# Kernel optimization log

Measured on AMD Instinct MI355X. Metric: run time of the kernel, lower is better.

Reference implementation:

```python
import jax, jax.numpy as jnp
import numpy as np
import math

B, L, C_IN = 64, 3168, 64
D_MODEL, K = 512, 16  # K = cycle_length (kernel width == stride)
W = L // K            # 198 output tokens from deform conv


def _positional(S, d, dtype):
    # PositionalEmbedding buffer, rows [0, S)
    pos = jnp.arange(S, dtype=jnp.float32)[:, None]
    div = jnp.exp(jnp.arange(0, d, 2, dtype=jnp.float32) * (-math.log(10000.0) / d))
    pe = jnp.zeros((S, d), jnp.float32)
    pe = pe.at[:, 0::2].set(jnp.sin(pos * div))
    pe = pe.at[:, 1::2].set(jnp.cos(pos * div))
    return pe.astype(dtype)


def setup_inputs() -> dict:
    key = jax.random.key(0)
    ks = jax.random.split(key, 6)
    fan_in = C_IN * K
    std = math.sqrt(2.0 / (1 + 0.01 ** 2) / fan_in)  # kaiming_normal, leaky_relu fan_in
    return {
        "x": jax.random.normal(ks[0], (B, L, C_IN), jnp.float32),
        "w_off": jax.random.normal(ks[1], (2 * K, C_IN, K), jnp.float32) * std,
        "b_off": jax.random.normal(ks[2], (2 * K,), jnp.float32) * 0.02,
        "w_def": jax.random.normal(ks[3], (D_MODEL, C_IN, K), jnp.float32) * std,
        "b_def": jax.random.normal(ks[4], (D_MODEL,), jnp.float32) * 0.02,
        "cls_token": jax.random.normal(ks[5], (1, 1, D_MODEL), jnp.float32),
    }


def _gather_cols(xt, idx, L_):
    # xt: (B, C, L); idx: (B, K, W) int32 -> (B, C, K, W), zero out-of-bounds
    b, c = xt.shape[0], xt.shape[1]
    valid = (idx >= 0) & (idx < L_)
    idxc = jnp.clip(idx, 0, L_ - 1).reshape(b, 1, -1)
    g = jnp.take_along_axis(xt, jnp.broadcast_to(idxc, (b, c, idxc.shape[-1])), axis=2)
    g = g.reshape(b, c, idx.shape[1], idx.shape[2])
    return jnp.where(valid[:, None], g, 0.0)


def reference(x, w_off, b_off, w_def, b_def, cls_token):
    b, l, c = x.shape
    w = l // K
    # offset conv: kernel (1,K), stride (1,K) == non-overlapping windows
    xr = x[:, : w * K, :].reshape(b, w, K, c)              # (B, W, K, C)
    off = jnp.einsum('bwkc,ock->bow', xr, w_off) + b_off[None, :, None]  # (B, 2K, W)
    dy = off[:, 0::2]                                      # (B, K, W)
    dx = off[:, 1::2]
    # sampling positions along width (height is size 1, base y = 0)
    base = (jnp.arange(w)[None, :] * K + jnp.arange(K)[:, None]).astype(x.dtype)  # (K, W)
    px = base[None] + dx                                   # (B, K, W)
    x0 = jnp.floor(px)
    frac = px - x0
    x0i = x0.astype(jnp.int32)
    xt = x.transpose(0, 2, 1)                              # (B, C, L)
    v0 = _gather_cols(xt, x0i, l)
    v1 = _gather_cols(xt, x0i + 1, l)
    wy = jnp.maximum(0.0, 1.0 - jnp.abs(dy))               # vertical bilinear weight on row 0
    val = wy[:, None] * ((1.0 - frac)[:, None] * v0 + frac[:, None] * v1)  # (B, C, K, W)
    out = jnp.einsum('bckw,dck->bwd', val, w_def) + b_def  # (B, W, d_model)
    tok = jnp.concatenate([jnp.broadcast_to(cls_token, (b, 1, D_MODEL)), out], axis=1)
    pe = _positional(w + 1, D_MODEL, tok.dtype)
    return tok + pe[None]
```

## Files before the change

### kernel.cpp

```cpp
#include <hip/hip_runtime.h>
#include <math.h>
#include <stdint.h>

#define NB 64
#define NL 3168
#define NC 64
#define ND 512
#define NK 16
#define NW 198
#define NM 12672
#define KD 1024

typedef __attribute__((ext_vector_type(8))) short bf8_t;
typedef __attribute__((ext_vector_type(4))) float f4_t;

typedef const unsigned int __attribute__((address_space(1)))* as1_u32p;
typedef unsigned int __attribute__((address_space(3)))* as3_u32p;

__device__ __forceinline__ void gl_lds16(const void* g, void* l) {
  __builtin_amdgcn_global_load_lds((as1_u32p)(uintptr_t)g,
                                   (as3_u32p)(unsigned int)(uintptr_t)l, 16, 0, 0);
}

__device__ __forceinline__ unsigned short f2bf(float f) {
  union { float f; unsigned u; } v; v.f = f;
  unsigned r = v.u + 0x7FFFu + ((v.u >> 16) & 1u);
  return (unsigned short)(r >> 16);
}

__global__ void prep_kernel(const float* __restrict__ w_off, const float* __restrict__ w_def,
                            const float* __restrict__ cls, unsigned short* __restrict__ wofft,
                            unsigned short* __restrict__ wdeft, float* __restrict__ pe,
                            float* __restrict__ out) {
  int id = blockIdx.x * 256 + threadIdx.x;
  if (id < 131072) {
    float4 v = ((const float4*)w_def)[id];
    ushort4 o;
    o.x = f2bf(v.x); o.y = f2bf(v.y); o.z = f2bf(v.z); o.w = f2bf(v.w);
    ((ushort4*)wdeft)[id] = o;
    return;
  }
  id -= 131072;
  if (id < 32768) {
    int o = id >> 10, kc = id & 1023, k = kc >> 6, c = kc & 63;
    wofft[id] = f2bf(w_off[o * 1024 + c * 16 + k]);
    return;
  }
  id -= 32768;
  if (id < 101888) {
    int pos = id >> 9, d = id & 511;
    int i = d >> 1;
    float freq = expf((float)(2 * i) * (-9.210340371976184f / 512.0f));
    float arg = (float)pos * freq;
    pe[id] = (d & 1) ? cosf(arg) : sinf(arg);
    return;
  }
  id -= 101888;
  {
    int b = id >> 9, d = id & 511;
    out[(size_t)(b * 199) * 512 + d] = cls[d] + ((d & 1) ? 1.0f : 0.0f);
  }
}

__launch_bounds__(512, 2)
__global__ void offsample_kernel(const float* __restrict__ x,
                                 const unsigned short* __restrict__ wofft,
                                 const float* __restrict__ b_off,
                                 unsigned short* __restrict__ val_ws) {
  __shared__ float partial[8][16][33];
  __shared__ float2 s_w[16][16];
  __shared__ int2   s_i[16][16];
  __shared__ int    s_base[16];
  int tid = threadIdx.x;
  int lane = tid & 63, wid = tid >> 6;
  int r16 = lane & 15, kg = lane >> 4;
  int flat = blockIdx.x;
  int bsw = (flat & 7) * 99 + (flat >> 3);
  int row0 = bsw * 16;

  f4_t acc[2] = {};
  const float* arow = x + (size_t)(row0 + r16) * KD + wid * 128;
  const unsigned short* bcol0 = wofft + r16 * KD + wid * 128;
  const unsigned short* bcol1 = wofft + (16 + r16) * KD + wid * 128;

#pragma unroll
  for (int ks = 0; ks < 4; ++ks) {
    int k0 = ks * 32 + kg * 8;
    float4 v0 = *(const float4*)(arow + k0);
    float4 v1 = *(const float4*)(arow + k0 + 4);
    bf8_t a;
    a[0] = (short)f2bf(v0.x); a[1] = (short)f2bf(v0.y);
    a[2] = (short)f2bf(v0.z); a[3] = (short)f2bf(v0.w);
    a[4] = (short)f2bf(v1.x); a[5] = (short)f2bf(v1.y);
    a[6] = (short)f2bf(v1.z); a[7] = (short)f2bf(v1.w);
    bf8_t b0 = *(const bf8_t*)(bcol0 + k0);
    bf8_t b1 = *(const bf8_t*)(bcol1 + k0);
    acc[0] = __builtin_amdgcn_mfma_f32_16x16x32_bf16(a, b0, acc[0], 0, 0, 0);
    acc[1] = __builtin_amdgcn_mfma_f32_16x16x32_bf16(a, b1, acc[1], 0, 0, 0);
  }
#pragma unroll
  for (int n = 0; n < 2; ++n)
#pragma unroll
    for (int r = 0; r < 4; ++r)
      partial[wid][kg * 4 + r][n * 16 + r16] = acc[n][r];
  __syncthreads();

  if (tid < 256) {
    int rp = tid >> 4, k = tid & 15;
    float dy = b_off[2 * k], dx = b_off[2 * k + 1];
#pragma unroll
    for (int w8 = 0; w8 < 8; ++w8) {
      dy += partial[w8][rp][2 * k];
      dx += partial[w8][rp][2 * k + 1];
    }
    int rg = row0 + rp;
    int b = rg / NW, w = rg - b * NW;
    if (k == 0) s_base[rp] = b * (NL * NC);
    float wy = fmaxf(0.f, 1.f - fabsf(dy));
    float px = (float)(w * 16 + k) + dx;
    float x0f = floorf(px);
    float frac = px - x0f;
    int x0 = (int)x0f;
    float w0 = wy * (1.f - frac), w1 = wy * frac;
    if (x0 < 0 || x0 >= NL) w0 = 0.f;
    if (x0 + 1 < 0 || x0 + 1 >= NL) w1 = 0.f;
    int x0c = min(max(x0, 0), NL - 1);
    int x1c = min(max(x0 + 1, 0), NL - 1);
    s_w[rp][k] = make_float2(w0, w1);
    s_i[rp][k] = make_int2(x0c * 64, x1c * 64);
  }
  __syncthreads();

#pragma unroll
  for (int rr = 0; rr < 2; ++rr) {
    int rp = wid * 2 + rr;
    const float* xb = x + s_base[rp];
    float v0[16], v1[16];
    float2 wk[16];
#pragma unroll
    for (int k = 0; k < 16; ++k) {
      int2 ik = s_i[rp][k];
      wk[k] = s_w[rp][k];
      v0[k] = xb[ik.x + lane];
      v1[k] = xb[ik.y + lane];
    }
    unsigned short vv[16];
#pragma unroll
    for (int k = 0; k < 16; ++k)
      vv[k] = f2bf(wk[k].x * v0[k] + wk[k].y * v1[k]);
    unsigned int p[8];
#pragma unroll
    for (int i = 0; i < 8; ++i)
      p[i] = (unsigned int)vv[2 * i] | ((unsigned int)vv[2 * i + 1] << 16);
    int rg = row0 + rp;
    uint4* dst = (uint4*)(val_ws + (size_t)rg * KD + lane * 16);
    dst[0] = make_uint4(p[0], p[1], p[2], p[3]);
    dst[1] = make_uint4(p[4], p[5], p[6], p[7]);
  }
}

__launch_bounds__(128)
__global__ void gemm_kernel(const unsigned short* __restrict__ val_ws,
                            const unsigned short* __restrict__ wdeft,
                            const float* __restrict__ b_def, const float* __restrict__ pe,
                            float* __restrict__ out) {
  __shared__ unsigned short As[2][128 * 64];
  __shared__ unsigned short Bs[2][64 * 64];
  int tid = threadIdx.x;
  int flat = blockIdx.x;
  int w = (flat & 7) * 99 + (flat >> 3);
  int mt = w >> 3, nt = w & 7;
  int lane = tid & 63, wid = tid >> 6;
  int r16 = lane & 15, kg = lane >> 4;
  f4_t acc[4][4] = {};

  int r_st = lane >> 3;
  int j_st = lane & 7;
  const char* aBase = (const char*)val_ws + (size_t)mt * 128 * 2048;
  const char* bBase = (const char*)wdeft + (size_t)nt * 64 * 2048;

  auto STAGE = [&](int ks, int buf) {
#pragma unroll
    for (int i = 0; i < 8; ++i) {
      int seg = wid * 8 + i;
      int r = seg * 8 + r_st;
      int src_off = ((j_st ^ (r & 7)) << 4);
      gl_lds16(aBase + (size_t)r * 2048 + ks * 128 + src_off, &As[buf][seg * 512]);
    }
#pragma unroll
    for (int i = 0; i < 4; ++i) {
      int seg = wid * 4 + i;
      int r = seg * 8 + r_st;
      int src_off = ((j_st ^ (r & 7)) << 4);
      gl_lds16(bBase + (size_t)r * 2048 + ks * 128 + src_off, &Bs[buf][seg * 512]);
    }
  };

  auto COMPUTE = [&](int buf) {
#pragma unroll
    for (int jb = 0; jb < 8; jb += 4) {
      bf8_t af[4], bf[4];
#pragma unroll
      for (int m = 0; m < 4; ++m) {
        int R = wid * 64 + m * 16 + r16;
        af[m] = *(const bf8_t*)&As[buf][R * 64 + (((jb + kg) ^ (R & 7)) << 3)];
      }
#pragma unroll
      for (int n = 0; n < 4; ++n) {
        int Rc = n * 16 + r16;
        bf[n] = *(const bf8_t*)&Bs[buf][Rc * 64 + (((jb + kg) ^ (Rc & 7)) << 3)];
      }
#pragma unroll
      for (int m = 0; m < 4; ++m)
#pragma unroll
        for (int n = 0; n < 4; ++n)
          acc[m][n] = __builtin_amdgcn_mfma_f32_16x16x32_bf16(af[m], bf[n], acc[m][n], 0, 0, 0);
    }
  };

  STAGE(0, 0);
  asm volatile("s_waitcnt vmcnt(0)" ::: "memory");
  __builtin_amdgcn_s_barrier();
#pragma unroll
  for (int t = 0; t < 16; ++t) {
    if (t < 15) {
      STAGE(t + 1, (t + 1) & 1);
      asm volatile("s_waitcnt vmcnt(12)" ::: "memory");
    } else {
      asm volatile("s_waitcnt vmcnt(0)" ::: "memory");
    }
    __builtin_amdgcn_s_barrier();
    COMPUTE(t & 1);
    asm volatile("s_waitcnt lgkmcnt(0)" ::: "memory");
    __builtin_amdgcn_sched_barrier(0);
    __builtin_amdgcn_s_barrier();
  }

#pragma unroll
  for (int m = 0; m < 4; ++m)
#pragma unroll
    for (int n = 0; n < 4; ++n)
#pragma unroll
      for (int r = 0; r < 4; ++r) {
        int grow = mt * 128 + wid * 64 + m * 16 + kg * 4 + r;
        int gcol = nt * 64 + n * 16 + r16;
        int bi = grow / NW, wi = grow - bi * NW;
        out[((size_t)(bi * 199 + wi + 1)) * 512 + gcol] =
            acc[m][n][r] + b_def[gcol] + pe[(wi + 1) * 512 + gcol];
      }
}

extern "C" void kernel_launch(void* const* d_in, const int* in_sizes, int n_in,
                              void* d_out, int out_size, void* d_ws, size_t ws_size,
                              hipStream_t stream) {
  const float* x     = (const float*)d_in[0];
  const float* w_off = (const float*)d_in[1];
  const float* b_off = (const float*)d_in[2];
  const float* w_def = (const float*)d_in[3];
  const float* b_def = (const float*)d_in[4];
  const float* cls   = (const float*)d_in[5];
  float* out = (float*)d_out;
  char* ws = (char*)d_ws;
  unsigned short* val_ws = (unsigned short*)ws;
  unsigned short* wofft  = (unsigned short*)(ws + 25952256);
  unsigned short* wdeft  = (unsigned short*)(ws + 26017792);
  float* pe              = (float*)(ws + 27066368);

  prep_kernel<<<1166, 256, 0, stream>>>(w_off, w_def, cls, wofft, wdeft, pe, out);
  offsample_kernel<<<NM / 16, 512, 0, stream>>>(x, wofft, b_off, val_ws);
  gemm_kernel<<<792, 128, 0, stream>>>(val_ws, wdeft, b_def, pe, out);
}
```

Measured before the change: 61.24 us.

## Replace double-buffered LDS pipeline in GEMM with single-buffer synchronous loop

Removes the two-stage LDS ping-pong in the GEMM kernel, where the next K-slice was prefetched with manual vmcnt waits while the current one was computed. Each K step now loads its tile into a single buffer between two __syncthreads and then computes. This halves LDS use per block, which can let more blocks share a CU. It gives up the overlap of global-to-LDS loads with MFMA work within a block. Correctness relies on __syncthreads waiting for the async global_load_lds transfers to finish.

```diff
diff --git a/kernel.cpp b/kernel.cpp
--- a/kernel.cpp
+++ b/kernel.cpp
@@ -164,8 +164,8 @@
                             const unsigned short* __restrict__ wdeft,
                             const float* __restrict__ b_def, const float* __restrict__ pe,
                             float* __restrict__ out) {
-  __shared__ unsigned short As[2][128 * 64];
-  __shared__ unsigned short Bs[2][64 * 64];
+  __shared__ unsigned short As[128 * 64];
+  __shared__ unsigned short Bs[64 * 64];
   int tid = threadIdx.x;
   int flat = blockIdx.x;
   int w = (flat & 7) * 99 + (flat >> 3);
@@ -179,36 +179,35 @@
   const char* aBase = (const char*)val_ws + (size_t)mt * 128 * 2048;
   const char* bBase = (const char*)wdeft + (size_t)nt * 64 * 2048;
 
-  auto STAGE = [&](int ks, int buf) {
+  for (int ks = 0; ks < 16; ++ks) {
+    __syncthreads();
 #pragma unroll
     for (int i = 0; i < 8; ++i) {
       int seg = wid * 8 + i;
       int r = seg * 8 + r_st;
       int src_off = ((j_st ^ (r & 7)) << 4);
-      gl_lds16(aBase + (size_t)r * 2048 + ks * 128 + src_off, &As[buf][seg * 512]);
+      gl_lds16(aBase + (size_t)r * 2048 + ks * 128 + src_off, &As[seg * 512]);
     }
 #pragma unroll
     for (int i = 0; i < 4; ++i) {
       int seg = wid * 4 + i;
       int r = seg * 8 + r_st;
       int src_off = ((j_st ^ (r & 7)) << 4);
-      gl_lds16(bBase + (size_t)r * 2048 + ks * 128 + src_off, &Bs[buf][seg * 512]);
-    }
-  };
-
-  auto COMPUTE = [&](int buf) {
+      gl_lds16(bBase + (size_t)r * 2048 + ks * 128 + src_off, &Bs[seg * 512]);
+    }
+    __syncthreads();
 #pragma unroll
     for (int jb = 0; jb < 8; jb += 4) {
       bf8_t af[4], bf[4];
 #pragma unroll
       for (int m = 0; m < 4; ++m) {
         int R = wid * 64 + m * 16 + r16;
-        af[m] = *(const bf8_t*)&As[buf][R * 64 + (((jb + kg) ^ (R & 7)) << 3)];
+        af[m] = *(const bf8_t*)&As[R * 64 + (((jb + kg) ^ (R & 7)) << 3)];
       }
 #pragma unroll
       for (int n = 0; n < 4; ++n) {
         int Rc = n * 16 + r16;
-        bf[n] = *(const bf8_t*)&Bs[buf][Rc * 64 + (((jb + kg) ^ (Rc & 7)) << 3)];
+        bf[n] = *(const bf8_t*)&Bs[Rc * 64 + (((jb + kg) ^ (Rc & 7)) << 3)];
       }
 #pragma unroll
       for (int m = 0; m < 4; ++m)
@@ -216,24 +215,6 @@
         for (int n = 0; n < 4; ++n)
           acc[m][n] = __builtin_amdgcn_mfma_f32_16x16x32_bf16(af[m], bf[n], acc[m][n], 0, 0, 0);
     }
-  };
-
-  STAGE(0, 0);
-  asm volatile("s_waitcnt vmcnt(0)" ::: "memory");
-  __builtin_amdgcn_s_barrier();
-#pragma unroll
-  for (int t = 0; t < 16; ++t) {
-    if (t < 15) {
-      STAGE(t + 1, (t + 1) & 1);
-      asm volatile("s_waitcnt vmcnt(12)" ::: "memory");
-    } else {
-      asm volatile("s_waitcnt vmcnt(0)" ::: "memory");
-    }
-    __builtin_amdgcn_s_barrier();
-    COMPUTE(t & 1);
-    asm volatile("s_waitcnt lgkmcnt(0)" ::: "memory");
-    __builtin_amdgcn_sched_barrier(0);
-    __builtin_amdgcn_s_barrier();
   }
 
 #pragma unroll
```

Result: no change. 61.26 us (+0.0%).
